# Kernel tuning notes

Hardware: AMD Instinct MI355X
Metric: run time of the kernel (lower is better)

## Reference

```python
import jax, jax.numpy as jnp
import numpy as np

DIM = 1024
NUM_HEAD = 16
DIM_HEAD = DIM // NUM_HEAD
MAX_SEQ_LEN = 4096
RMS_EPS = 1.1920928955078125e-07  # torch nn.RMSNorm default eps = finfo(fp32).eps
LIN_EPS = 1e-6
PAD_VAL = 1.0
THETA = 10000.0


def rmsnorm(x, g):
    return x * jax.lax.rsqrt(jnp.mean(x * x, axis=-1, keepdims=True) + RMS_EPS) * g


def setup_inputs() -> dict:
    key = jax.random.key(0)
    ks = jax.random.split(key, 20)
    B, L, C, D = 4, 2048, 256, DIM
    s = 1.0 / np.sqrt(D)
    inp = {
        "x": jax.random.normal(ks[0], (B, L, D), jnp.float32),
        "context": jax.random.normal(ks[1], (B, C, D), jnp.float32),
        "attn_mask": jax.random.randint(ks[2], (B, L, L), 0, 2).astype(bool),
        "start_pos": jax.random.randint(ks[3], (B,), 0, MAX_SEQ_LEN - L).astype(jnp.int64),
        "Wqkv": jax.random.normal(ks[4], (D, 3 * D), jnp.float32) * s,
        "bqkv": jax.random.normal(ks[5], (3 * D,), jnp.float32) * 0.01,
        "g_q": jnp.ones((D,), jnp.float32),
        "g_k": jnp.ones((D,), jnp.float32),
        "cWqkv": jax.random.normal(ks[6], (D, 3 * D), jnp.float32) * s,
        "cbqkv": jax.random.normal(ks[7], (3 * D,), jnp.float32) * 0.01,
        "cg_q": jnp.ones((D,), jnp.float32),
        "cg_k": jnp.ones((D,), jnp.float32),
        "Wout": jax.random.normal(ks[8], (D, D), jnp.float32) * s,
        "bout": jax.random.normal(ks[9], (D,), jnp.float32) * 0.01,
        "g_out": jnp.ones((D,), jnp.float32),
        "cWout": jax.random.normal(ks[10], (D, D), jnp.float32) * s,
        "cbout": jax.random.normal(ks[11], (D,), jnp.float32) * 0.01,
        "cg_out": jnp.ones((D,), jnp.float32),
    }
    return inp


def _freqs(pos_indices):
    # pos_indices: (B, L) int
    inv = 1.0 / (THETA ** (jnp.arange(0, DIM_HEAD, 2, dtype=jnp.float32) / DIM_HEAD))  # (DH/2,)
    ang = pos_indices.astype(jnp.float32)[..., None] * inv  # (B, L, DH/2)
    return jnp.cos(ang), jnp.sin(ang)


def _apply_rope(t, cos, sin):
    # t: (B, H, L, DH); cos/sin: (B, L, DH/2) -> broadcast over head
    B, H, L, DH = t.shape
    tr = t.reshape(B, H, L, DH // 2, 2)
    t0, t1 = tr[..., 0], tr[..., 1]
    c = cos[:, None]  # (B,1,L,DH/2)
    s = sin[:, None]
    out = jnp.stack([t0 * c - t1 * s, t0 * s + t1 * c], axis=-1)
    return out.reshape(B, H, L, DH)


def _split_heads(t):
    B, L, D = t.shape
    return t.reshape(B, L, NUM_HEAD, DIM_HEAD).transpose(0, 2, 1, 3)


def _augment_mask(m, C):
    # m: (B, L, L) bool -> (B, L+C, L+C) bool
    B, L, _ = m.shape
    c_to_seq = jnp.broadcast_to(jnp.any(m, axis=1, keepdims=True), (B, C, L))
    seq_to_c = jnp.broadcast_to(jnp.any(m, axis=2, keepdims=True), (B, L, C))
    c_to_c = jnp.ones((B, C, C), bool)
    top = jnp.concatenate([m, seq_to_c], axis=2)
    bot = jnp.concatenate([c_to_seq, c_to_c], axis=2)
    return jnp.concatenate([top, bot], axis=1)


def reference(x, context, attn_mask, start_pos, Wqkv, bqkv, g_q, g_k,
              cWqkv, cbqkv, cg_q, cg_k, Wout, bout, g_out, cWout, cbout, cg_out):
    B, L, D = x.shape
    C = context.shape[1]

    q, k, v = jnp.split(x @ Wqkv + bqkv, 3, axis=-1)
    q = rmsnorm(q, g_q)
    k = rmsnorm(k, g_k)
    q, k, v = _split_heads(q), _split_heads(k), _split_heads(v)  # (B,H,L,DH)

    pos = start_pos[:, None] + jnp.arange(L, dtype=start_pos.dtype)[None]  # (B,L)
    cos, sin = _freqs(pos)
    q = _apply_rope(q, cos, sin)
    k = _apply_rope(k, cos, sin)

    cq, ck, cv = jnp.split(context @ cWqkv + cbqkv, 3, axis=-1)
    cq = rmsnorm(cq, cg_q)
    ck = rmsnorm(ck, cg_k)
    cq, ck, cv = _split_heads(cq), _split_heads(ck), _split_heads(cv)

    q = jnp.concatenate([q, cq], axis=2)  # (B,H,S,DH), S=L+C
    k = jnp.concatenate([k, ck], axis=2)
    v = jnp.concatenate([v, cv], axis=2)

    full_mask = _augment_mask(attn_mask, C)[:, None]  # (B,1,S,S)

    # linear attention: ReLU feature map + padded-value trick
    qf = jax.nn.relu(q)
    kf = jax.nn.relu(k)
    k_mask = full_mask[:, :, 0, :][..., None].astype(kf.dtype)  # (B,1,S,1)
    kf = kf * k_mask
    vpad = jnp.pad(v, ((0, 0), (0, 0), (0, 0), (0, 1)), constant_values=PAD_VAL)  # (B,H,S,DH+1)
    vk = jnp.einsum('bhse,bhsd->bhed', vpad, kf)        # (B,H,DH+1,DH)
    res = jnp.einsum('bhed,bhqd->bhqe', vk, qf)          # (B,H,S,DH+1)
    attn = res[..., :-1] / (res[..., -1:] + LIN_EPS)     # (B,H,S,DH)

    attn = attn.transpose(0, 2, 1, 3).reshape(B, L + C, D)
    x_out = rmsnorm(attn[:, :L] @ Wout + bout, g_out)
    c_out = rmsnorm(attn[:, L:] @ cWout + cbout, cg_out)
    return x_out, c_out
```

## Files before the change

kernel.cpp:

```cpp
#include <hip/hip_runtime.h>

typedef __bf16 bf16;
typedef __bf16 bf16x4 __attribute__((ext_vector_type(4)));
typedef __bf16 bf16x8 __attribute__((ext_vector_type(8)));
typedef float  floatx4 __attribute__((ext_vector_type(4)));

#define L_SEQ   2048
#define C_SEQ   256
#define S_SEQ   2304
#define NBATCH  4
#define NHEAD   16
#define DHEAD   64
#define DMODEL  1024
#define RMS_EPS 1.1920928955078125e-07f
#define LIN_EPS 1e-6f

__device__ __forceinline__ void gload_lds16(const void* g, void* l) {
  __builtin_amdgcn_global_load_lds(
      (const __attribute__((address_space(1))) void*)g,
      (__attribute__((address_space(3))) void*)l, 16, 0, 0);
}

__device__ __forceinline__ void transpose_job(
    const float* __restrict__ src, bf16* __restrict__ dst,
    int R, int C, int tb, bf16 (*tile)[33]) {
  int tilesx = C >> 5;
  int c0 = (tb % tilesx) * 32, r0 = (tb / tilesx) * 32;
  int tx = threadIdx.x & 31, ty = threadIdx.x >> 5;
  for (int i = ty; i < 32; i += 8)
    tile[i][tx] = (bf16)src[(size_t)(r0 + i) * C + c0 + tx];
  __syncthreads();
  for (int i = ty; i < 32; i += 8)
    dst[(size_t)(c0 + i) * R + r0 + tx] = tile[tx][i];
}

__device__ __forceinline__ void convert_job(
    const float* __restrict__ src, bf16* __restrict__ dst, int tb) {
  size_t i = ((size_t)tb * 256 + threadIdx.x) * 8;
  floatx4 a = *(const floatx4*)(src + i);
  floatx4 b = *(const floatx4*)(src + i + 4);
  bf16x8 o;
#pragma unroll
  for (int j = 0; j < 4; j++) { o[j] = (bf16)a[j]; o[4 + j] = (bf16)b[j]; }
  *(bf16x8*)(dst + i) = o;
}

__global__ __launch_bounds__(256) void prep(
    const float* __restrict__ Wqkv, const float* __restrict__ cWqkv,
    const float* __restrict__ Wout, const float* __restrict__ cWout,
    const float* __restrict__ x, const float* __restrict__ ctx,
    const int* __restrict__ mask, const int* __restrict__ spos,
    bf16* __restrict__ WqkvT, bf16* __restrict__ cWqkvT,
    bf16* __restrict__ WoutT, bf16* __restrict__ cWoutT,
    bf16* __restrict__ xbf, bf16* __restrict__ cbf,
    float* __restrict__ vkw, float* __restrict__ rope,
    int* __restrict__ anym) {
  __shared__ bf16 tile[32][33];
  __shared__ int sh;
  int b = blockIdx.x;
  if (b < 3072) { transpose_job(Wqkv, WqkvT, 1024, 3072, b, tile); return; }
  b -= 3072;
  if (b < 3072) { transpose_job(cWqkv, cWqkvT, 1024, 3072, b, tile); return; }
  b -= 3072;
  if (b < 1024) { transpose_job(Wout, WoutT, 1024, 1024, b, tile); return; }
  b -= 1024;
  if (b < 1024) { transpose_job(cWout, cWoutT, 1024, 1024, b, tile); return; }
  b -= 1024;
  if (b < 4096) { convert_job(x, xbf, b); return; }
  b -= 4096;
  if (b < 512) { convert_job(ctx, cbf, b); return; }
  b -= 512;
  if (b < 260) {
    int i = b * 1024 + threadIdx.x * 4;
    *(floatx4*)(vkw + i) = floatx4{0.f, 0.f, 0.f, 0.f};
    return;
  }
  b -= 260;
  if (b < 2048) {
    int t = threadIdx.x;
    int tok = b * 4 + (t >> 6);
    int bb = tok >> 11, s = tok & 2047;
    int j = t & 63, fi = j >> 1;
    float ang = (float)(spos[bb] + s) * expf((float)fi * -0.28782313662425572f);
    rope[(size_t)tok * 64 + j] = (j & 1) ? sinf(ang) : cosf(ang);
    return;
  }
  b -= 2048;
  int a = 0;
  size_t base = (size_t)b * L_SEQ * L_SEQ;
  for (int j = threadIdx.x; j < L_SEQ; j += 256) a |= mask[base + j];
  if (threadIdx.x == 0) sh = 0;
  __syncthreads();
  if (a) atomicOr(&sh, 1);
  __syncthreads();
  if (threadIdx.x == 0) anym[b] = sh;
}

template <bool SCATTER>
__global__ __launch_bounds__(512, 2) void gemm_bias(
    const bf16* __restrict__ A1, const bf16* __restrict__ A2,
    const bf16* __restrict__ B1t, const bf16* __restrict__ B2t,
    const float* __restrict__ bias1, const float* __restrict__ bias2,
    bf16* __restrict__ C1, bf16* __restrict__ C2,
    bf16* __restrict__ qs, bf16* __restrict__ ks, bf16* __restrict__ vs,
    int N, int K, int ybound,
    int rpb1, int soff1, int rpb2, int soff2) {
  __shared__ bf16 As[2][16384];
  __shared__ bf16 Bs[2][16384];

  int nwg = gridDim.x * gridDim.y;
  int wg = blockIdx.y * gridDim.x + blockIdx.x;
  int cpx = nwg >> 3;
  wg = (wg & 7) * cpx + (wg >> 3);
  int bx = wg % gridDim.x, by = wg / gridDim.x;
  int n0 = bx * 256;
  const bf16 *Ap, *Bt;
  const float* bias;
  bf16* Cp;
  int m0, rpb, soff;
  if (by < ybound) {
    Ap = A1; Bt = B1t; bias = bias1; Cp = C1;
    m0 = by * 256; rpb = rpb1; soff = soff1;
  } else {
    Ap = A2; Bt = B2t; bias = bias2; Cp = C2;
    m0 = (by - ybound) * 256; rpb = rpb2; soff = soff2;
  }

  int t = threadIdx.x, lane = t & 63, w = t >> 6;
  int wr = w >> 2, wc = w & 3;
  int l16 = lane & 15, l4 = lane >> 4;

  int srow = w * 32 + (lane >> 3);
  int scol = ((lane & 7) ^ (lane >> 3)) << 3;
  const bf16* Ab = Ap + (size_t)(m0 + srow) * K + scol;
  const bf16* Bb = Bt + (size_t)(n0 + srow) * K + scol;

  int co0 = (l4 * 8) ^ ((l16 & 7) << 3);
  int co1 = (32 + l4 * 8) ^ ((l16 & 7) << 3);
  int rba = (wr * 128 + l16) * 64;
  int rbb = (wc * 64 + l16) * 64;

  floatx4 acc[8][4] = {};

#pragma unroll
  for (int j = 0; j < 4; j++) {
    gload_lds16(Ab + (size_t)j * 8 * K, (char*)As + w * 4096 + j * 1024);
    gload_lds16(Bb + (size_t)j * 8 * K, (char*)Bs + w * 4096 + j * 1024);
  }
  __syncthreads();

  int NT = K >> 6;
  for (int tt = 0; tt < NT; ++tt) {
    int p = tt & 1;
    if (tt + 1 < NT) {
      int kb = (tt + 1) << 6;
#pragma unroll
      for (int j = 0; j < 4; j++) {
        gload_lds16(Ab + (size_t)j * 8 * K + kb,
                    (char*)As + (p ^ 1) * 32768 + w * 4096 + j * 1024);
        gload_lds16(Bb + (size_t)j * 8 * K + kb,
                    (char*)Bs + (p ^ 1) * 32768 + w * 4096 + j * 1024);
      }
    }
    const bf16* Asp = As[p];
    const bf16* Bsp = Bs[p];
    bf16x8 b0[4], b1[4];
#pragma unroll
    for (int nt = 0; nt < 4; nt++) {
      b0[nt] = *(const bf16x8*)&Bsp[rbb + nt * 1024 + co0];
      b1[nt] = *(const bf16x8*)&Bsp[rbb + nt * 1024 + co1];
    }
    __builtin_amdgcn_s_setprio(1);
#pragma unroll
    for (int mt = 0; mt < 8; mt++) {
      bf16x8 a0 = *(const bf16x8*)&Asp[rba + mt * 1024 + co0];
      bf16x8 a1 = *(const bf16x8*)&Asp[rba + mt * 1024 + co1];
#pragma unroll
      for (int nt = 0; nt < 4; nt++) {
        acc[mt][nt] = __builtin_amdgcn_mfma_f32_16x16x32_bf16(a0, b0[nt], acc[mt][nt], 0, 0, 0);
        acc[mt][nt] = __builtin_amdgcn_mfma_f32_16x16x32_bf16(a1, b1[nt], acc[mt][nt], 0, 0, 0);
      }
    }
    __builtin_amdgcn_s_setprio(0);
    __syncthreads();
  }

#pragma unroll
  for (int mt = 0; mt < 8; mt++)
#pragma unroll
    for (int nt = 0; nt < 4; nt++) {
      int col = n0 + wc * 64 + nt * 16 + l16;
      float bval = bias[col];
      if constexpr (SCATTER) {
        int which = col >> 10;
        int h = (col >> 6) & 15;
        int dh = col & 63;
        int rmask = (1 << rpb) - 1;
        if (which == 2) {
          int rw0 = m0 + wr * 128 + mt * 16 + l4 * 4;
          int b = rw0 >> rpb;
          int s = soff + (rw0 & rmask);
          bf16x4 o;
#pragma unroll
          for (int r = 0; r < 4; r++) o[r] = (bf16)(acc[mt][nt][r] + bval);
          *(bf16x4*)(vs + ((size_t)(b * NHEAD + h) * DHEAD + dh) * S_SEQ + s) = o;
        } else {
          bf16* dst = which == 0 ? qs : ks;
#pragma unroll
          for (int r = 0; r < 4; r++) {
            int rw = m0 + wr * 128 + mt * 16 + l4 * 4 + r;
            int b = rw >> rpb;
            int s = soff + (rw & rmask);
            dst[((size_t)(b * NHEAD + h) * S_SEQ + s) * DHEAD + dh] =
                (bf16)(acc[mt][nt][r] + bval);
          }
        }
      } else {
#pragma unroll
        for (int r = 0; r < 4; r++) {
          int rw = m0 + wr * 128 + mt * 16 + l4 * 4 + r;
          Cp[(size_t)rw * N + col] = (bf16)(acc[mt][nt][r] + bval);
        }
      }
    }
}

__global__ __launch_bounds__(256) void qkv_post(
    bf16* __restrict__ qs, bf16* __restrict__ ks,
    const int* __restrict__ mask, const float* __restrict__ rope,
    const int* __restrict__ anym,
    const float* __restrict__ g_q, const float* __restrict__ g_k,
    const float* __restrict__ cg_q, const float* __restrict__ cg_k) {
  int g = blockIdx.x, t = threadIdx.x;
  bool is_ctx = g >= NBATCH * L_SEQ;
  int b, s;
  const float *gq, *gk;
  float mval;
  if (!is_ctx) {
    b = g >> 11;
    int l = g & 2047;
    s = l;
    mval = mask[(size_t)b * L_SEQ * L_SEQ + l] ? 1.f : 0.f;
    gq = g_q; gk = g_k;
  } else {
    int gg = g - NBATCH * L_SEQ;
    b = gg >> 8;
    s = L_SEQ + (gg & 255);
    mval = anym[b] ? 1.f : 0.f;
    gq = cg_q; gk = cg_k;
  }
  int d0 = t * 4;
  int h = t >> 4, dh = (t & 15) * 4;
  size_t base = ((size_t)(b * NHEAD + h) * S_SEQ + s) * DHEAD + dh;
  bf16x4 q4 = *(const bf16x4*)(qs + base);
  bf16x4 k4 = *(const bf16x4*)(ks + base);
  float qv[4], kv[4], pq = 0.f, pk = 0.f;
#pragma unroll
  for (int i = 0; i < 4; i++) {
    qv[i] = (float)q4[i]; kv[i] = (float)k4[i];
    pq += qv[i] * qv[i];  pk += kv[i] * kv[i];
  }
  int lane = t & 63, w = t >> 6;
  for (int off = 32; off > 0; off >>= 1) {
    pq += __shfl_down(pq, off, 64);
    pk += __shfl_down(pk, off, 64);
  }
  __shared__ float red[8];
  if (lane == 0) { red[w] = pq; red[4 + w] = pk; }
  __syncthreads();
  float sq = red[0] + red[1] + red[2] + red[3];
  float sk = red[4] + red[5] + red[6] + red[7];
  float scq = rsqrtf(sq * (1.f / DMODEL) + RMS_EPS);
  float sck = rsqrtf(sk * (1.f / DMODEL) + RMS_EPS);
#pragma unroll
  for (int i = 0; i < 4; i++) {
    qv[i] *= scq * gq[d0 + i];
    kv[i] *= sck * gk[d0 + i];
  }
  if (!is_ctx) {
    floatx4 tb4 = *(const floatx4*)&rope[((size_t)(b << 11 | s)) * 64 + dh];
#pragma unroll
    for (int pr = 0; pr < 2; pr++) {
      float cc = tb4[2 * pr], ss = tb4[2 * pr + 1];
      float t0 = qv[2 * pr], t1 = qv[2 * pr + 1];
      qv[2 * pr]     = t0 * cc - t1 * ss;
      qv[2 * pr + 1] = t0 * ss + t1 * cc;
      t0 = kv[2 * pr]; t1 = kv[2 * pr + 1];
      kv[2 * pr]     = t0 * cc - t1 * ss;
      kv[2 * pr + 1] = t0 * ss + t1 * cc;
    }
  }
  bf16x4 qo, ko;
#pragma unroll
  for (int i = 0; i < 4; i++) {
    qo[i] = (bf16)fmaxf(qv[i], 0.f);
    ko[i] = (bf16)(fmaxf(kv[i], 0.f) * mval);
  }
  *(bf16x4*)(qs + base) = qo;
  *(bf16x4*)(ks + base) = ko;
}

#define VK_CH   8
#define VK_SPAN (S_SEQ / VK_CH)
__global__ __launch_bounds__(256) void vk_mfma(
    const bf16* __restrict__ vT, const bf16* __restrict__ kf,
    float* __restrict__ vk) {
  __shared__ bf16 Vs[2][64][40];
  __shared__ bf16 Ks[2][64][40];
  int bh = blockIdx.x >> 3, chunk = blockIdx.x & 7;
  int t = threadIdx.x, lane = t & 63, w = t >> 6;
  int l16 = lane & 15, l4 = lane >> 4;
  const bf16* vp = vT + (size_t)bh * DHEAD * S_SEQ;
  const bf16* kp = kf + (size_t)bh * S_SEQ * DHEAD;
  int s_begin = chunk * VK_SPAN;
  int ve = t >> 2, vso = (t & 3) * 8;
  int ks_s = t & 31, kd0 = (t >> 5) * 8;
  floatx4 acc[4] = {};
  float dsum[8] = {};
  bf16x8 vv = *(const bf16x8*)(vp + (size_t)ve * S_SEQ + s_begin + vso);
  bf16x8 kv = *(const bf16x8*)(kp + (size_t)(s_begin + ks_s) * DHEAD + kd0);
  for (int st = 0; st < VK_SPAN; st += 32) {
    int cur = (st >> 5) & 1;
    *(bf16x8*)&Vs[cur][ve][vso] = vv;
#pragma unroll
    for (int j = 0; j < 8; j++) {
      Ks[cur][kd0 + j][ks_s] = kv[j];
      dsum[j] += (float)kv[j];
    }
    if (st + 32 < VK_SPAN) {
      int s0 = s_begin + st + 32;
      vv = *(const bf16x8*)(vp + (size_t)ve * S_SEQ + s0 + vso);
      kv = *(const bf16x8*)(kp + (size_t)(s0 + ks_s) * DHEAD + kd0);
    }
    __syncthreads();
    bf16x8 af = *(const bf16x8*)&Vs[cur][w * 16 + l16][l4 * 8];
#pragma unroll
    for (int nt = 0; nt < 4; nt++) {
      bf16x8 bfr = *(const bf16x8*)&Ks[cur][nt * 16 + l16][l4 * 8];
      acc[nt] = __builtin_amdgcn_mfma_f32_16x16x32_bf16(af, bfr, acc[nt], 0, 0, 0);
    }
  }
  float* vkbh = vk + (size_t)bh * 65 * 64;
#pragma unroll
  for (int nt = 0; nt < 4; nt++)
#pragma unroll
    for (int r = 0; r < 4; r++)
      atomicAdd(&vkbh[(w * 16 + l4 * 4 + r) * 64 + nt * 16 + l16], acc[nt][r]);
#pragma unroll
  for (int j = 0; j < 8; j++)
#pragma unroll
    for (int off = 16; off > 0; off >>= 1)
      dsum[j] += __shfl_down(dsum[j], off, 32);
  if ((lane & 31) == 0)
#pragma unroll
    for (int j = 0; j < 8; j++)
      atomicAdd(&vkbh[64 * 64 + kd0 + j], dsum[j]);
}

__global__ __launch_bounds__(256) void res_attn(
    const bf16* __restrict__ qf, const float* __restrict__ vk,
    bf16* __restrict__ attn_x, bf16* __restrict__ attn_c) {
  __shared__ bf16 Bs[80][72];
  __shared__ float sden[256];
  int bh = blockIdx.x / 9, mblk = blockIdx.x % 9;
  int b = bh >> 4, h = bh & 15;
  int t = threadIdx.x, lane = t & 63, w = t >> 6;
  const float* vkp = vk + (size_t)bh * 65 * 64;
  for (int i = t; i < 80 * 64; i += 256) {
    int e = i >> 6, d = i & 63;
    Bs[e][d] = (bf16)(e < 65 ? vkp[i] : 0.f);
  }
  __syncthreads();
  int l16 = lane & 15, l4 = lane >> 4;
  const bf16* qbase = qf + (size_t)bh * S_SEQ * DHEAD;
  int q0w = mblk * 256 + w * 64;

  floatx4 acc[4][5] = {};
  bf16x8 af[4][2], bfr[5][2];
#pragma unroll
  for (int mt = 0; mt < 4; mt++) {
    int q = q0w + mt * 16 + l16;
    af[mt][0] = *(const bf16x8*)(qbase + (size_t)q * 64 + l4 * 8);
    af[mt][1] = *(const bf16x8*)(qbase + (size_t)q * 64 + 32 + l4 * 8);
  }
#pragma unroll
  for (int nt = 0; nt < 5; nt++) {
    bfr[nt][0] = *(const bf16x8*)&Bs[nt * 16 + l16][l4 * 8];
    bfr[nt][1] = *(const bf16x8*)&Bs[nt * 16 + l16][32 + l4 * 8];
  }
#pragma unroll
  for (int mt = 0; mt < 4; mt++)
#pragma unroll
    for (int nt = 0; nt < 5; nt++) {
      acc[mt][nt] = __builtin_amdgcn_mfma_f32_16x16x32_bf16(af[mt][0], bfr[nt][0], acc[mt][nt], 0, 0, 0);
      acc[mt][nt] = __builtin_amdgcn_mfma_f32_16x16x32_bf16(af[mt][1], bfr[nt][1], acc[mt][nt], 0, 0, 0);
    }
  if (l16 == 0) {
#pragma unroll
    for (int mt = 0; mt < 4; mt++)
#pragma unroll
      for (int r = 0; r < 4; r++)
        sden[w * 64 + mt * 16 + l4 * 4 + r] = acc[mt][4][r];
  }
  __syncthreads();
#pragma unroll
  for (int mt = 0; mt < 4; mt++)
#pragma unroll
    for (int r = 0; r < 4; r++) {
      float den = sden[w * 64 + mt * 16 + l4 * 4 + r] + LIN_EPS;
      float rden = 1.f / den;
      int q = q0w + mt * 16 + l4 * 4 + r;
#pragma unroll
      for (int nt = 0; nt < 4; nt++) {
        int dcol = nt * 16 + l16;
        float a = acc[mt][nt][r] * rden;
        if (q < L_SEQ)
          attn_x[((size_t)b * L_SEQ + q) * DMODEL + h * DHEAD + dcol] = (bf16)a;
        else
          attn_c[((size_t)b * C_SEQ + (q - L_SEQ)) * DMODEL + h * DHEAD + dcol] = (bf16)a;
      }
    }
}

__global__ __launch_bounds__(256) void final_norm(
    const bf16* __restrict__ y_x, const bf16* __restrict__ y_c,
    const float* __restrict__ g_out, const float* __restrict__ cg_out,
    float* __restrict__ out) {
  int g = blockIdx.x, t = threadIdx.x;
  const bf16* src;
  const float* gv;
  if (g < NBATCH * L_SEQ) {
    src = y_x + (size_t)g * DMODEL; gv = g_out;
  } else {
    int gg = g - NBATCH * L_SEQ;
    src = y_c + (size_t)gg * DMODEL; gv = cg_out;
  }
  float* dst = out + (size_t)g * DMODEL;
  int d0 = t * 4;
  bf16x4 y4 = *(const bf16x4*)(src + d0);
  float yv[4], p = 0.f;
#pragma unroll
  for (int i = 0; i < 4; i++) { yv[i] = (float)y4[i]; p += yv[i] * yv[i]; }
  int lane = t & 63, w = t >> 6;
  for (int off = 32; off > 0; off >>= 1) p += __shfl_down(p, off, 64);
  __shared__ float red[4];
  if (lane == 0) red[w] = p;
  __syncthreads();
  float ssum = red[0] + red[1] + red[2] + red[3];
  float sc = rsqrtf(ssum * (1.f / DMODEL) + RMS_EPS);
  floatx4 o;
#pragma unroll
  for (int i = 0; i < 4; i++) o[i] = yv[i] * sc * gv[d0 + i];
  *(floatx4*)(dst + d0) = o;
}

extern "C" void kernel_launch(void* const* d_in, const int* in_sizes, int n_in,
                              void* d_out, int out_size, void* d_ws, size_t ws_size,
                              hipStream_t stream) {
  const float* x      = (const float*)d_in[0];
  const float* ctx    = (const float*)d_in[1];
  const int*   mask   = (const int*)d_in[2];
  const int*   spos   = (const int*)d_in[3];
  const float* Wqkv   = (const float*)d_in[4];
  const float* bqkv   = (const float*)d_in[5];
  const float* g_q    = (const float*)d_in[6];
  const float* g_k    = (const float*)d_in[7];
  const float* cWqkv  = (const float*)d_in[8];
  const float* cbqkv  = (const float*)d_in[9];
  const float* cg_q   = (const float*)d_in[10];
  const float* cg_k   = (const float*)d_in[11];
  const float* Wout   = (const float*)d_in[12];
  const float* bout   = (const float*)d_in[13];
  const float* g_out  = (const float*)d_in[14];
  const float* cWout  = (const float*)d_in[15];
  const float* cbout  = (const float*)d_in[16];
  const float* cg_out = (const float*)d_in[17];

  char* wsp = (char*)d_ws;
  size_t off = 0;
  auto alloc = [&](size_t bytes) -> void* {
    void* p = wsp + off;
    off += (bytes + 255) & ~(size_t)255;
    return p;
  };
  bf16* WqkvT  = (bf16*)alloc((size_t)3072 * 1024 * 2);
  bf16* cWqkvT = (bf16*)alloc((size_t)3072 * 1024 * 2);
  bf16* WoutT  = (bf16*)alloc((size_t)1024 * 1024 * 2);
  bf16* cWoutT = (bf16*)alloc((size_t)1024 * 1024 * 2);
  bf16* xbf    = (bf16*)alloc((size_t)NBATCH * L_SEQ * DMODEL * 2);
  bf16* cbf    = (bf16*)alloc((size_t)NBATCH * C_SEQ * DMODEL * 2);
  const size_t SLAB = (size_t)NBATCH * NHEAD * S_SEQ * DHEAD;
  bf16* qfs    = (bf16*)alloc(SLAB * 2);
  bf16* kfs    = (bf16*)alloc(SLAB * 2);
  bf16* vfs    = (bf16*)alloc(SLAB * 2);
  float* vkw   = (float*)alloc((size_t)64 * 65 * 64 * 4);
  float* rope  = (float*)alloc((size_t)NBATCH * L_SEQ * 64 * 4);
  int* anym    = (int*)alloc(256);
  bf16* attn_x = kfs;
  bf16* attn_c = kfs + (size_t)NBATCH * L_SEQ * DMODEL;
  bf16* y_x    = vfs;
  bf16* y_c    = vfs + (size_t)NBATCH * L_SEQ * DMODEL;

  prep<<<15112, 256, 0, stream>>>(Wqkv, cWqkv, Wout, cWout, x, ctx, mask, spos,
                                  WqkvT, cWqkvT, WoutT, cWoutT, xbf, cbf,
                                  vkw, rope, anym);

  gemm_bias<true><<<dim3(12, 36), 512, 0, stream>>>(
      xbf, cbf, WqkvT, cWqkvT, bqkv, cbqkv, nullptr, nullptr,
      qfs, kfs, vfs, 3072, 1024, 32, 11, 0, 8, L_SEQ);

  qkv_post<<<NBATCH * (L_SEQ + C_SEQ), 256, 0, stream>>>(
      qfs, kfs, mask, rope, anym, g_q, g_k, cg_q, cg_k);

  vk_mfma<<<64 * VK_CH, 256, 0, stream>>>(vfs, kfs, vkw);

  res_attn<<<576, 256, 0, stream>>>(qfs, vkw, attn_x, attn_c);

  gemm_bias<false><<<dim3(4, 36), 512, 0, stream>>>(
      attn_x, attn_c, WoutT, cWoutT, bout, cbout, y_x, y_c,
      nullptr, nullptr, nullptr, 1024, 1024, 32, 0, 0, 0, 0);

  final_norm<<<NBATCH * (L_SEQ + C_SEQ), 256, 0, stream>>>(
      y_x, y_c, g_out, cg_out, (float*)d_out);
}
```

Before: 350.3 us.

## Halve GEMM K-tile, add 128x128 tile variant for output projection, more vk chunks

The bf16 GEMM now stages K in 32-wide slices instead of 64, which halves the LDS footprint and changes the swizzle and fragment loads. A template flag adds a 128x128-tile, 256-thread variant, used for the output projection so it launches four times as many workgroups. The launch-bounds occupancy hint is raised for both variants. Separately, the vk reduction splits the sequence into 12 chunks instead of 8 for more parallelism. The risks are more barrier iterations per GEMM and register pressure from the higher occupancy hint on the 256-tile path, which could cause spills.

```diff
diff --git a/kernel.cpp b/kernel.cpp
--- a/kernel.cpp
+++ b/kernel.cpp
@@ -96,8 +96,8 @@
   if (threadIdx.x == 0) anym[b] = sh;
 }
 
-template <bool SCATTER>
-__global__ __launch_bounds__(512, 2) void gemm_bias(
+template <bool SCATTER, bool T256>
+__global__ __launch_bounds__(T256 ? 512 : 256, 4) void gemm_bias(
     const bf16* __restrict__ A1, const bf16* __restrict__ A2,
     const bf16* __restrict__ B1t, const bf16* __restrict__ B2t,
     const float* __restrict__ bias1, const float* __restrict__ bias2,
@@ -105,88 +105,77 @@
     bf16* __restrict__ qs, bf16* __restrict__ ks, bf16* __restrict__ vs,
     int N, int K, int ybound,
     int rpb1, int soff1, int rpb2, int soff2) {
-  __shared__ bf16 As[2][16384];
-  __shared__ bf16 Bs[2][16384];
+  constexpr int BMv = T256 ? 256 : 128;
+  constexpr int MT  = T256 ? 8 : 4;
+  constexpr int WRS = T256 ? 128 : 64;
+  __shared__ bf16 As[2][BMv * 32];
+  __shared__ bf16 Bs[2][BMv * 32];
 
   int nwg = gridDim.x * gridDim.y;
   int wg = blockIdx.y * gridDim.x + blockIdx.x;
   int cpx = nwg >> 3;
   wg = (wg & 7) * cpx + (wg >> 3);
   int bx = wg % gridDim.x, by = wg / gridDim.x;
-  int n0 = bx * 256;
+  int n0 = bx * BMv;
   const bf16 *Ap, *Bt;
   const float* bias;
   bf16* Cp;
   int m0, rpb, soff;
   if (by < ybound) {
     Ap = A1; Bt = B1t; bias = bias1; Cp = C1;
-    m0 = by * 256; rpb = rpb1; soff = soff1;
+    m0 = by * BMv; rpb = rpb1; soff = soff1;
   } else {
     Ap = A2; Bt = B2t; bias = bias2; Cp = C2;
-    m0 = (by - ybound) * 256; rpb = rpb2; soff = soff2;
+    m0 = (by - ybound) * BMv; rpb = rpb2; soff = soff2;
   }
 
   int t = threadIdx.x, lane = t & 63, w = t >> 6;
-  int wr = w >> 2, wc = w & 3;
+  int wr, wc;
+  if constexpr (T256) { wr = w >> 2; wc = w & 3; }
+  else                { wr = w >> 1; wc = w & 1; }
   int l16 = lane & 15, l4 = lane >> 4;
 
-  int srow = w * 32 + (lane >> 3);
-  int scol = ((lane & 7) ^ (lane >> 3)) << 3;
-  const bf16* Ab = Ap + (size_t)(m0 + srow) * K + scol;
-  const bf16* Bb = Bt + (size_t)(n0 + srow) * K + scol;
-
-  int co0 = (l4 * 8) ^ ((l16 & 7) << 3);
-  int co1 = (32 + l4 * 8) ^ ((l16 & 7) << 3);
-  int rba = (wr * 128 + l16) * 64;
-  int rbb = (wc * 64 + l16) * 64;
-
-  floatx4 acc[8][4] = {};
-
-#pragma unroll
-  for (int j = 0; j < 4; j++) {
-    gload_lds16(Ab + (size_t)j * 8 * K, (char*)As + w * 4096 + j * 1024);
-    gload_lds16(Bb + (size_t)j * 8 * K, (char*)Bs + w * 4096 + j * 1024);
-  }
-  __syncthreads();
-
-  int NT = K >> 6;
-  for (int tt = 0; tt < NT; ++tt) {
+  int crow = w * 32 + (lane >> 2);
+  int scol = (((lane & 3) ^ ((lane >> 2) & 3)) << 3);
+  const bf16* Ab = Ap + (size_t)(m0 + crow) * K + scol;
+  const bf16* Bb = Bt + (size_t)(n0 + crow) * K + scol;
+
+  auto stage = [&](int buf, int kb) {
+#pragma unroll
+    for (int j = 0; j < 2; j++) {
+      gload_lds16(Ab + (size_t)(j * 16) * K + kb, (char*)As[buf] + (w * 2 + j) * 1024);
+      gload_lds16(Bb + (size_t)(j * 16) * K + kb, (char*)Bs[buf] + (w * 2 + j) * 1024);
+    }
+  };
+
+  int co = (l4 * 8) ^ ((l16 & 3) << 3);
+  int rba = (wr * WRS + l16) * 32 + co;
+  int rbb = (wc * 64 + l16) * 32 + co;
+
+  floatx4 acc[MT][4] = {};
+  stage(0, 0);
+  __syncthreads();
+  int NTt = K >> 5;
+  for (int tt = 0; tt < NTt; ++tt) {
     int p = tt & 1;
-    if (tt + 1 < NT) {
-      int kb = (tt + 1) << 6;
-#pragma unroll
-      for (int j = 0; j < 4; j++) {
-        gload_lds16(Ab + (size_t)j * 8 * K + kb,
-                    (char*)As + (p ^ 1) * 32768 + w * 4096 + j * 1024);
-        gload_lds16(Bb + (size_t)j * 8 * K + kb,
-                    (char*)Bs + (p ^ 1) * 32768 + w * 4096 + j * 1024);
-      }
-    }
-    const bf16* Asp = As[p];
-    const bf16* Bsp = Bs[p];
-    bf16x8 b0[4], b1[4];
-#pragma unroll
-    for (int nt = 0; nt < 4; nt++) {
-      b0[nt] = *(const bf16x8*)&Bsp[rbb + nt * 1024 + co0];
-      b1[nt] = *(const bf16x8*)&Bsp[rbb + nt * 1024 + co1];
-    }
+    if (tt + 1 < NTt) stage(p ^ 1, (tt + 1) << 5);
+    bf16x8 bfr[4];
+#pragma unroll
+    for (int nt = 0; nt < 4; nt++) bfr[nt] = *(const bf16x8*)&Bs[p][rbb + nt * 512];
     __builtin_amdgcn_s_setprio(1);
 #pragma unroll
-    for (int mt = 0; mt < 8; mt++) {
-      bf16x8 a0 = *(const bf16x8*)&Asp[rba + mt * 1024 + co0];
-      bf16x8 a1 = *(const bf16x8*)&Asp[rba + mt * 1024 + co1];
-#pragma unroll
-      for (int nt = 0; nt < 4; nt++) {
-        acc[mt][nt] = __builtin_amdgcn_mfma_f32_16x16x32_bf16(a0, b0[nt], acc[mt][nt], 0, 0, 0);
-        acc[mt][nt] = __builtin_amdgcn_mfma_f32_16x16x32_bf16(a1, b1[nt], acc[mt][nt], 0, 0, 0);
-      }
+    for (int mt = 0; mt < MT; mt++) {
+      bf16x8 a = *(const bf16x8*)&As[p][rba + mt * 512];
+#pragma unroll
+      for (int nt = 0; nt < 4; nt++)
+        acc[mt][nt] = __builtin_amdgcn_mfma_f32_16x16x32_bf16(a, bfr[nt], acc[mt][nt], 0, 0, 0);
     }
     __builtin_amdgcn_s_setprio(0);
     __syncthreads();
   }
 
 #pragma unroll
-  for (int mt = 0; mt < 8; mt++)
+  for (int mt = 0; mt < MT; mt++)
 #pragma unroll
     for (int nt = 0; nt < 4; nt++) {
       int col = n0 + wc * 64 + nt * 16 + l16;
@@ -197,7 +186,7 @@
         int dh = col & 63;
         int rmask = (1 << rpb) - 1;
         if (which == 2) {
-          int rw0 = m0 + wr * 128 + mt * 16 + l4 * 4;
+          int rw0 = m0 + wr * WRS + mt * 16 + l4 * 4;
           int b = rw0 >> rpb;
           int s = soff + (rw0 & rmask);
           bf16x4 o;
@@ -208,7 +197,7 @@
           bf16* dst = which == 0 ? qs : ks;
 #pragma unroll
           for (int r = 0; r < 4; r++) {
-            int rw = m0 + wr * 128 + mt * 16 + l4 * 4 + r;
+            int rw = m0 + wr * WRS + mt * 16 + l4 * 4 + r;
             int b = rw >> rpb;
             int s = soff + (rw & rmask);
             dst[((size_t)(b * NHEAD + h) * S_SEQ + s) * DHEAD + dh] =
@@ -218,7 +207,7 @@
       } else {
 #pragma unroll
         for (int r = 0; r < 4; r++) {
-          int rw = m0 + wr * 128 + mt * 16 + l4 * 4 + r;
+          int rw = m0 + wr * WRS + mt * 16 + l4 * 4 + r;
           Cp[(size_t)rw * N + col] = (bf16)(acc[mt][nt][r] + bval);
         }
       }
@@ -300,14 +289,14 @@
   *(bf16x4*)(ks + base) = ko;
 }
 
-#define VK_CH   8
+#define VK_CH   12
 #define VK_SPAN (S_SEQ / VK_CH)
 __global__ __launch_bounds__(256) void vk_mfma(
     const bf16* __restrict__ vT, const bf16* __restrict__ kf,
     float* __restrict__ vk) {
   __shared__ bf16 Vs[2][64][40];
   __shared__ bf16 Ks[2][64][40];
-  int bh = blockIdx.x >> 3, chunk = blockIdx.x & 7;
+  int bh = blockIdx.x / VK_CH, chunk = blockIdx.x % VK_CH;
   int t = threadIdx.x, lane = t & 63, w = t >> 6;
   int l16 = lane & 15, l4 = lane >> 4;
   const bf16* vp = vT + (size_t)bh * DHEAD * S_SEQ;
@@ -505,7 +494,7 @@
                                   WqkvT, cWqkvT, WoutT, cWoutT, xbf, cbf,
                                   vkw, rope, anym);
 
-  gemm_bias<true><<<dim3(12, 36), 512, 0, stream>>>(
+  gemm_bias<true, true><<<dim3(12, 36), 512, 0, stream>>>(
       xbf, cbf, WqkvT, cWqkvT, bqkv, cbqkv, nullptr, nullptr,
       qfs, kfs, vfs, 3072, 1024, 32, 11, 0, 8, L_SEQ);
 
@@ -516,9 +505,9 @@
 
   res_attn<<<576, 256, 0, stream>>>(qfs, vkw, attn_x, attn_c);
 
-  gemm_bias<false><<<dim3(4, 36), 512, 0, stream>>>(
+  gemm_bias<false, false><<<dim3(8, 72), 256, 0, stream>>>(
       attn_x, attn_c, WoutT, cWoutT, bout, cbout, y_x, y_c,
-      nullptr, nullptr, nullptr, 1024, 1024, 32, 0, 0, 0, 0);
+      nullptr, nullptr, nullptr, 1024, 1024, 64, 0, 0, 0, 0);
 
   final_norm<<<NBATCH * (L_SEQ + C_SEQ), 256, 0, stream>>>(
       y_x, y_c, g_out, cg_out, (float*)d_out);
```

Result: slower. 735.8 us (+110.0%).
